# Kernel tuning notes

Measured on AMD Instinct MI355X. Metric: run time of the kernel, lower is better.

Reference implementation:

```python
import jax, jax.numpy as jnp
import numpy as np

H = 8          # nhead
EPS_Z = 1e-6   # linear-attention normalizer eps
LN_EPS = 1e-5  # torch LayerNorm default


def _ln(x, g, b):
    m = x.mean(-1, keepdims=True)
    v = ((x - m) ** 2).mean(-1, keepdims=True)
    return (x - m) * jax.lax.rsqrt(v + LN_EPS) * g + b


def setup_inputs() -> dict:
    key = jax.random.key(0)
    ks = jax.random.split(key, 8)
    B, S, E, F = 4, 8192, 512, 2048
    s = 0.02
    return {
        "src": jax.random.normal(ks[0], (B, S, E), jnp.float32),
        "Wq": jax.random.normal(ks[1], (E, E), jnp.float32) * s,
        "bq": jnp.zeros((E,), jnp.float32),
        "Wk": jax.random.normal(ks[2], (E, E), jnp.float32) * s,
        "bk": jnp.zeros((E,), jnp.float32),
        "Wv": jax.random.normal(ks[3], (E, E), jnp.float32) * s,
        "bv": jnp.zeros((E,), jnp.float32),
        "Wo": jax.random.normal(ks[4], (E, E), jnp.float32) * s,
        "bo": jnp.zeros((E,), jnp.float32),
        "W1": jax.random.normal(ks[5], (E, F), jnp.float32) * s,
        "b1": jnp.zeros((F,), jnp.float32),
        "W2": jax.random.normal(ks[6], (F, E), jnp.float32) * s,
        "b2": jnp.zeros((E,), jnp.float32),
        "g1": jnp.ones((E,), jnp.float32),
        "be1": jnp.zeros((E,), jnp.float32),
        "g2": jnp.ones((E,), jnp.float32),
        "be2": jnp.zeros((E,), jnp.float32),
    }


def reference(src, Wq, bq, Wk, bk, Wv, bv, Wo, bo, W1, b1, W2, b2, g1, be1, g2, be2):
    B, S, E = src.shape
    Dh = E // H

    def heads(x):  # [B,S,E] -> [B,H,S,Dh]
        return x.reshape(B, S, H, Dh).transpose(0, 2, 1, 3)

    q = heads(src @ Wq + bq)
    k = heads(src @ Wk + bk)
    v = heads(src @ Wv + bv)

    qm = jax.nn.elu(q) + 1.0  # feature map: ELU+1
    km = jax.nn.elu(k) + 1.0

    kv = jnp.einsum("bhsd,bhse->bhde", km, v)          # [B,H,Dh,Dh]
    ksum = km.sum(axis=2)                               # [B,H,Dh]
    z = 1.0 / (jnp.einsum("bhsd,bhd->bhs", qm, ksum) + EPS_Z)
    attn = jnp.einsum("bhsd,bhde->bhse", qm, kv) * z[..., None]

    attn = attn.transpose(0, 2, 1, 3).reshape(B, S, E) @ Wo + bo
    x = _ln(src + attn, g1, be1)
    ff = jax.nn.relu(x @ W1 + b1) @ W2 + b2
    return _ln(x + ff, g2, be2)
```

## Files before the change

### kernel.cpp

```cpp
#include <hip/hip_runtime.h>
#include <hip/hip_bf16.h>

typedef __attribute__((ext_vector_type(8))) short bf16x8;
typedef __attribute__((ext_vector_type(4))) float f32x4;

__device__ inline ushort f2bf(float f) {
    uint u = __float_as_uint(f);
    u += 0x7fff + ((u >> 16) & 1);
    return (ushort)(u >> 16);
}
__device__ inline float bf2f(ushort h) {
    return __uint_as_float(((uint)h) << 16);
}

__device__ inline void gload16(const void* g, void* lds) {
    __builtin_amdgcn_global_load_lds(
        (const __attribute__((address_space(1))) void*)g,
        (__attribute__((address_space(3))) void*)lds, 16, 0, 0);
}

__global__ __launch_bounds__(256) void prep(
    const float* __restrict__ src, ushort* __restrict__ src16,
    const float* __restrict__ Wq, const float* __restrict__ Wk,
    const float* __restrict__ Wv, const float* __restrict__ Wo,
    const float* __restrict__ W1, const float* __restrict__ W2,
    ushort* __restrict__ wqkv, ushort* __restrict__ wot,
    ushort* __restrict__ w1t, ushort* __restrict__ w2t,
    const float* __restrict__ bq, const float* __restrict__ bk,
    const float* __restrict__ bv, float* __restrict__ bqkv) {
    __shared__ float tile[32][33];
    int bid = blockIdx.x;
    const int t = threadIdx.x;
    if (bid < 16384) {
        int i = bid * 256 + t;
        float4 a = ((const float4*)src)[i];
        ushort4 o;
        o.x = f2bf(a.x); o.y = f2bf(a.y); o.z = f2bf(a.z); o.w = f2bf(a.w);
        ((ushort4*)src16)[i] = o;
        return;
    }
    bid -= 16384;
    const float* in; ushort* out; int Kd, Nd;
    if (bid < 1024) {
        int m = bid >> 8;
        in = (m == 0) ? Wq : (m == 1) ? Wk : (m == 2) ? Wv : Wo;
        out = (m == 3) ? wot : (wqkv + m * 512 * 512);
        Kd = 512; Nd = 512; bid &= 255;
    } else if (bid < 2048) { in = W1; out = w1t; Kd = 512; Nd = 2048; bid -= 1024; }
    else if (bid < 3072) { in = W2; out = w2t; Kd = 2048; Nd = 512; bid -= 2048; }
    else {
        int i = (bid - 3072) * 256 + t;
        if (i < 512) bqkv[i] = bq[i];
        else if (i < 1024) bqkv[i] = bk[i - 512];
        else if (i < 1536) bqkv[i] = bv[i - 1024];
        return;
    }
    const int nx = Nd / 32;
    const int nbase = (bid % nx) * 32, kb = (bid / nx) * 32;
    const int tx = t & 31, ty = t >> 5;
#pragma unroll
    for (int i = 0; i < 4; i++)
        tile[ty + i * 8][tx] = in[(size_t)(kb + ty + i * 8) * Nd + nbase + tx];
    __syncthreads();
#pragma unroll
    for (int i = 0; i < 4; i++) {
        int n = nbase + ty + i * 8, k = kb + tx;
        out[(size_t)n * Kd + k] = f2bf(tile[tx][ty + i * 8]);
    }
}

template <int EPI, int NT, int GB>
__global__ __launch_bounds__(512, 2) void gemm256(
    const ushort* __restrict__ A, const ushort* __restrict__ Bt,
    const float* __restrict__ bias, const ushort* __restrict__ res16,
    ushort* __restrict__ out16, int M, int N, int K, int nb1) {
    extern __shared__ char smem[];
    const int t = threadIdx.x;
    const int w = t >> 6, l = t & 63;
    const int wr = w >> 2, wc = w & 3;
    const int nwg = gridDim.x, cpx = nwg >> 3;
    const int swz = (blockIdx.x & 7) * cpx + (blockIdx.x >> 3);
    int bx0, by0;
    if (GB == 0) { bx0 = (swz % nb1) * NT; by0 = swz / nb1; }
    else         { bx0 = swz % nb1;        by0 = (swz / nb1) * NT; }

    const int scoff = ((t & 7) ^ ((t >> 3) & 7)) * 8;
    const ushort* pA = A + (size_t)(by0 * 256 + (t >> 3)) * K + scoff;
    const ushort* pB = Bt + (size_t)(bx0 * 256 + (t >> 3)) * K + scoff;
    const size_t u64K = (size_t)64 * K;

    const int Kt = K >> 6;
    const int TOT = NT * Kt;
    int skt = 0;
    size_t adv = 0;

#define STG8(buf)                                                              \
    {                                                                          \
        char* Lb = (buf) + (w << 10);                                          \
        _Pragma("unroll")                                                      \
        for (int u = 0; u < 4; ++u) {                                          \
            gload16(pA + (size_t)u * u64K + (GB ? adv : 0) + skt * 64,         \
                    Lb + u * 8192);                                            \
            gload16(pB + (size_t)u * u64K + (GB ? 0 : adv) + skt * 64,         \
                    Lb + 32768 + u * 8192);                                    \
        }                                                                      \
        if (++skt == Kt) { skt = 0; adv += (size_t)256 * K; }                  \
    }

    const int cA0 = ((l >> 4) ^ (l & 7)) * 16;
    const int cA1 = ((4 + (l >> 4)) ^ (l & 7)) * 16;
    const int baseA = (wr * 128 + (l & 15)) * 128;
    const int baseB = 32768 + (wc * 64 + (l & 15)) * 128;

    STG8(smem);

    f32x4 acc[8][4] = {};
    int g = 0;
    for (int j = 0; j < NT; ++j) {
#pragma unroll 1
        for (int kt = 0; kt < Kt; ++kt, ++g) {
            asm volatile("s_waitcnt vmcnt(0)" ::: "memory");
            __builtin_amdgcn_s_barrier();
            __builtin_amdgcn_sched_barrier(0);

            const char* cb = smem + (g & 1) * 65536;
            if (g + 1 < TOT) STG8(smem + ((g + 1) & 1) * 65536);

            bf16x8 a[8], b[4];
#pragma unroll
            for (int n = 0; n < 4; n++) b[n] = *(const bf16x8*)(cb + baseB + n * 2048 + cA0);
#pragma unroll
            for (int m = 0; m < 8; m++) a[m] = *(const bf16x8*)(cb + baseA + m * 2048 + cA0);
#pragma unroll
            for (int m = 0; m < 8; m++)
#pragma unroll
                for (int n = 0; n < 4; n++)
                    acc[m][n] = __builtin_amdgcn_mfma_f32_16x16x32_bf16(a[m], b[n], acc[m][n], 0, 0, 0);
#pragma unroll
            for (int n = 0; n < 4; n++) b[n] = *(const bf16x8*)(cb + baseB + n * 2048 + cA1);
#pragma unroll
            for (int m = 0; m < 8; m++) a[m] = *(const bf16x8*)(cb + baseA + m * 2048 + cA1);
#pragma unroll
            for (int m = 0; m < 8; m++)
#pragma unroll
                for (int n = 0; n < 4; n++)
                    acc[m][n] = __builtin_amdgcn_mfma_f32_16x16x32_bf16(a[m], b[n], acc[m][n], 0, 0, 0);
        }

        {
            const int bx = (GB == 0) ? (bx0 + j) : bx0;
            const int by = (GB == 0) ? by0 : (by0 + j);
            const int row0 = by * 256 + wr * 128 + ((l >> 4) << 2);
            const int col0 = bx * 256 + wc * 64 + (l & 15);
            const int seg = bx >> 1;
            const size_t segoff = (size_t)seg * M * 512;
            const int c511 = col0 & 511;
            float bv[4];
#pragma unroll
            for (int n = 0; n < 4; n++) bv[n] = bias[col0 + n * 16];
#pragma unroll
            for (int m = 0; m < 8; m++) {
#pragma unroll
                for (int r = 0; r < 4; r++) {
                    const int row = row0 + m * 16 + r;
                    const size_t base = (size_t)row * N + col0;
#pragma unroll
                    for (int n = 0; n < 4; n++) {
                        float vv = acc[m][n][r] + bv[n];
                        if constexpr (EPI == 2) {
                            vv = vv > 0.f ? vv : 0.f;
                            out16[base + n * 16] = f2bf(vv);
                        } else if constexpr (EPI == 3) {
                            vv += bf2f(res16[base + n * 16]);
                            out16[base + n * 16] = f2bf(vv);
                        } else if constexpr (EPI == 4) {
                            if (seg < 2) vv = vv > 0.f ? vv + 1.f : __expf(vv);
                            out16[segoff + (size_t)row * 512 + c511 + n * 16] = f2bf(vv);
                        } else {
                            out16[base + n * 16] = f2bf(vv);
                        }
                    }
                }
            }
            if (j + 1 < NT) {
#pragma unroll
                for (int m = 0; m < 8; m++)
#pragma unroll
                    for (int n = 0; n < 4; n++)
                        acc[m][n] = (f32x4){0.f, 0.f, 0.f, 0.f};
            }
        }
    }
#undef STG8
}

__global__ __launch_bounds__(256) void kv_partial(
    const ushort* __restrict__ km, const ushort* __restrict__ v,
    float* __restrict__ kvp, float* __restrict__ ksump, int S) {
    __shared__ ushort kms[32 * 64];
    __shared__ ushort vs[32 * 64];
    const int t = threadIdx.x;
    const int bh = blockIdx.y, b = bh >> 3, h = bh & 7;
    const int d0 = (t >> 4) * 4, e0 = (t & 15) * 4;
    float acc[4][4] = {};
    float ks = 0.f;
    const int s_base = blockIdx.x * 512;
    const int r = t >> 3, c8 = (t & 7) * 8;
    for (int s0 = 0; s0 < 512; s0 += 32) {
        size_t grow = ((size_t)b * S + s_base + s0 + r) * 512 + h * 64 + c8;
        *(uint4*)&kms[r * 64 + c8] = *(const uint4*)&km[grow];
        *(uint4*)&vs[r * 64 + c8] = *(const uint4*)&v[grow];
        __syncthreads();
#pragma unroll 4
        for (int s = 0; s < 32; ++s) {
            ushort4 ka = *(const ushort4*)&kms[s * 64 + d0];
            ushort4 vb = *(const ushort4*)&vs[s * 64 + e0];
            float a0 = bf2f(ka.x), a1 = bf2f(ka.y), a2 = bf2f(ka.z), a3 = bf2f(ka.w);
            float b0 = bf2f(vb.x), b1 = bf2f(vb.y), b2 = bf2f(vb.z), b3 = bf2f(vb.w);
            acc[0][0] += a0 * b0; acc[0][1] += a0 * b1; acc[0][2] += a0 * b2; acc[0][3] += a0 * b3;
            acc[1][0] += a1 * b0; acc[1][1] += a1 * b1; acc[1][2] += a1 * b2; acc[1][3] += a1 * b3;
            acc[2][0] += a2 * b0; acc[2][1] += a2 * b1; acc[2][2] += a2 * b2; acc[2][3] += a2 * b3;
            acc[3][0] += a3 * b0; acc[3][1] += a3 * b1; acc[3][2] += a3 * b2; acc[3][3] += a3 * b3;
            if (t < 64) ks += bf2f(kms[s * 64 + t]);
        }
        __syncthreads();
    }
    float* dst = kvp + ((size_t)bh * 16 + blockIdx.x) * 4096;
#pragma unroll
    for (int i = 0; i < 4; i++)
#pragma unroll
        for (int j = 0; j < 4; j++)
            dst[(d0 + i) * 64 + e0 + j] = acc[i][j];
    if (t < 64) ksump[((size_t)bh * 16 + blockIdx.x) * 64 + t] = ks;
}

__global__ void kv_reduce(const float* __restrict__ kvp, const float* __restrict__ ksump,
                          ushort* __restrict__ kvt, float* __restrict__ ksum) {
    int i = blockIdx.x * 256 + threadIdx.x;
    if (i < 32 * 4096) {
        int bh = i >> 12, de = i & 4095;
        int d = de >> 6, e = de & 63;
        float s = 0.f;
#pragma unroll
        for (int c = 0; c < 16; ++c) s += kvp[((size_t)bh * 16 + c) * 4096 + de];
        kvt[(size_t)bh * 4096 + e * 64 + d] = f2bf(s);
    } else {
        int j = i - 32 * 4096;
        if (j < 32 * 64) {
            int bh = j >> 6, d = j & 63;
            float s = 0.f;
#pragma unroll
            for (int c = 0; c < 16; ++c) s += ksump[((size_t)bh * 16 + c) * 64 + d];
            ksum[j] = s;
        }
    }
}

__global__ __launch_bounds__(256) void attn_mfma(
    const ushort* __restrict__ qm, const ushort* __restrict__ kvt,
    const float* __restrict__ ksum, ushort* __restrict__ attnE, int S) {
    __shared__ ushort As[128 * 128];
    __shared__ ushort Bs[128 * 64];
    __shared__ float zbuf[128][2];
    __shared__ float ks2[128];
    const int t = threadIdx.x, w = t >> 6, l = t & 63;
    const int cx = blockIdx.x, by = blockIdx.y;
    const int b = (by * 128) / S;
    const int h0 = cx * 2;
    const size_t arow0 = (size_t)(by * 128) * 512 + cx * 128;

#pragma unroll
    for (int rd = 0; rd < 8; ++rd) {
        const ushort* g = qm + arow0 + (size_t)(rd * 16 + w * 4 + (l >> 4)) * 512 + (l & 15) * 8;
        gload16(g, (char*)As + rd * 4096 + w * 1024);
    }
    const ushort* kvbase = kvt + (size_t)(b * 8 + h0) * 4096;
#pragma unroll
    for (int rd = 0; rd < 4; ++rd) {
        const ushort* g = kvbase + (rd * 32 + w * 8 + (l >> 3)) * 64 + (l & 7) * 8;
        gload16(g, (char*)Bs + rd * 4096 + w * 1024);
    }
    if (t < 128) ks2[t] = ksum[(b * 8 + h0) * 64 + t];
    __syncthreads();

    {
        const int r = t >> 1, hh = t & 1;
        float den = 0.f;
#pragma unroll
        for (int d0 = 0; d0 < 64; d0 += 8) {
            bf16x8 qv = *(const bf16x8*)&As[r * 128 + hh * 64 + d0];
#pragma unroll
            for (int j = 0; j < 8; j++) den += bf2f((ushort)qv[j]) * ks2[hh * 64 + d0 + j];
        }
        zbuf[r][hh] = 1.0f / (den + 1e-6f);
    }

    const int wr = w >> 1, wc = w & 1;
    const int ar = wr * 64 + (l & 15);
    const int br = wc * 64 + (l & 15);
    const int ko = (l >> 4) * 8;
    f32x4 acc[4][4] = {};
#pragma unroll
    for (int ks_ = 0; ks_ < 2; ++ks_) {
        bf16x8 a[4], bb[4];
#pragma unroll
        for (int m = 0; m < 4; m++)
            a[m] = *(const bf16x8*)&As[(ar + m * 16) * 128 + wc * 64 + ks_ * 32 + ko];
#pragma unroll
        for (int n = 0; n < 4; n++)
            bb[n] = *(const bf16x8*)&Bs[(br + n * 16) * 64 + ks_ * 32 + ko];
#pragma unroll
        for (int m = 0; m < 4; m++)
#pragma unroll
            for (int n = 0; n < 4; n++)
                acc[m][n] = __builtin_amdgcn_mfma_f32_16x16x32_bf16(a[m], bb[n], acc[m][n], 0, 0, 0);
    }
    __syncthreads();

    const int row0l = wr * 64 + ((l >> 4) << 2);
    ushort* outbase = attnE + (size_t)(by * 128) * 512 + cx * 128;
#pragma unroll
    for (int n = 0; n < 4; n++) {
#pragma unroll
        for (int m = 0; m < 4; m++) {
#pragma unroll
            for (int r = 0; r < 4; r++) {
                int rl = row0l + m * 16 + r;
                float z = zbuf[rl][wc];
                outbase[(size_t)rl * 512 + wc * 64 + n * 16 + (l & 15)] = f2bf(acc[m][n][r] * z);
            }
        }
    }
}

template <int OUT32>
__global__ __launch_bounds__(256) void ln_bf16(
    const ushort* __restrict__ in, const float* __restrict__ g, const float* __restrict__ be,
    void* __restrict__ outp, int Mrows) {
    const int w = threadIdx.x >> 6, l = threadIdx.x & 63;
    const int row = blockIdx.x * 4 + w;
    if (row >= Mrows) return;
    const ushort* rp = in + (size_t)row * 512;
    uint4 u = *(const uint4*)&rp[l * 8];
    float x[8];
    x[0] = bf2f((ushort)(u.x & 0xffff)); x[1] = bf2f((ushort)(u.x >> 16));
    x[2] = bf2f((ushort)(u.y & 0xffff)); x[3] = bf2f((ushort)(u.y >> 16));
    x[4] = bf2f((ushort)(u.z & 0xffff)); x[5] = bf2f((ushort)(u.z >> 16));
    x[6] = bf2f((ushort)(u.w & 0xffff)); x[7] = bf2f((ushort)(u.w >> 16));
    float s = 0.f, ss = 0.f;
#pragma unroll
    for (int j = 0; j < 8; j++) { s += x[j]; ss += x[j] * x[j]; }
#pragma unroll
    for (int o = 1; o < 64; o <<= 1) {
        s += __shfl_xor(s, o, 64);
        ss += __shfl_xor(ss, o, 64);
    }
    float mean = s * (1.f / 512.f);
    float var = ss * (1.f / 512.f) - mean * mean;
    float rstd = rsqrtf(var + 1e-5f);
    float4 g0 = *(const float4*)&g[l * 8], g1v = *(const float4*)&g[l * 8 + 4];
    float4 b0 = *(const float4*)&be[l * 8], b1v = *(const float4*)&be[l * 8 + 4];
    float o0[8];
    o0[0] = (x[0] - mean) * rstd * g0.x + b0.x;
    o0[1] = (x[1] - mean) * rstd * g0.y + b0.y;
    o0[2] = (x[2] - mean) * rstd * g0.z + b0.z;
    o0[3] = (x[3] - mean) * rstd * g0.w + b0.w;
    o0[4] = (x[4] - mean) * rstd * g1v.x + b1v.x;
    o0[5] = (x[5] - mean) * rstd * g1v.y + b1v.y;
    o0[6] = (x[6] - mean) * rstd * g1v.z + b1v.z;
    o0[7] = (x[7] - mean) * rstd * g1v.w + b1v.w;
    if constexpr (OUT32) {
        float* op = (float*)outp + (size_t)row * 512;
        *(float4*)&op[l * 8] = make_float4(o0[0], o0[1], o0[2], o0[3]);
        *(float4*)&op[l * 8 + 4] = make_float4(o0[4], o0[5], o0[6], o0[7]);
    } else {
        ushort* op = (ushort*)outp + (size_t)row * 512;
        ushort4 u0, u1;
        u0.x = f2bf(o0[0]); u0.y = f2bf(o0[1]); u0.z = f2bf(o0[2]); u0.w = f2bf(o0[3]);
        u1.x = f2bf(o0[4]); u1.y = f2bf(o0[5]); u1.z = f2bf(o0[6]); u1.w = f2bf(o0[7]);
        *(ushort4*)&op[l * 8] = u0;
        *(ushort4*)&op[l * 8 + 4] = u1;
    }
}

extern "C" void kernel_launch(void* const* d_in, const int* in_sizes, int n_in,
                              void* d_out, int out_size, void* d_ws, size_t ws_size,
                              hipStream_t stream) {
    const int B = 4, S = 8192, E = 512, F = 2048;
    const int M = B * S;
    const size_t SZ = (size_t)M * E * 2;
    const int SMEM = 131072;

    const float* src = (const float*)d_in[0];
    const float* Wq = (const float*)d_in[1];  const float* bq = (const float*)d_in[2];
    const float* Wk = (const float*)d_in[3];  const float* bk = (const float*)d_in[4];
    const float* Wv = (const float*)d_in[5];  const float* bv = (const float*)d_in[6];
    const float* Wo = (const float*)d_in[7];  const float* bo = (const float*)d_in[8];
    const float* W1 = (const float*)d_in[9];  const float* b1 = (const float*)d_in[10];
    const float* W2 = (const float*)d_in[11]; const float* b2 = (const float*)d_in[12];
    const float* g1 = (const float*)d_in[13]; const float* be1 = (const float*)d_in[14];
    const float* g2 = (const float*)d_in[15]; const float* be2 = (const float*)d_in[16];

    char* ws = (char*)d_ws;
    ushort* qm    = (ushort*)(ws + 0 * SZ);
    ushort* km    = (ushort*)(ws + 1 * SZ);
    ushort* v     = (ushort*)(ws + 2 * SZ);
    ushort* src16 = (ushort*)(ws + 3 * SZ);
    ushort* x16   = (ushort*)(ws + 4 * SZ);
    ushort* z16   = (ushort*)(ws + 5 * SZ);
    char*   tail  = ws + 6 * SZ;
    float*  kvp   = (float*)(tail);
    float*  ksump = (float*)(tail + 8388608);
    ushort* kvt   = (ushort*)(tail + 8519680);
    float*  ksum  = (float*)(tail + 8781824);
    float*  bqkv  = (float*)(tail + 8790016);
    ushort* wqkv  = (ushort*)(tail + 8796160);
    ushort* wot   = (ushort*)(tail + 10369024);
    ushort* w1t   = (ushort*)(tail + 10893312);
    ushort* w2t   = (ushort*)(tail + 12990464);
    ushort* attnE = km;
    ushort* y16   = v;
    ushort* hbuf  = (ushort*)(ws + 0);

    hipFuncSetAttribute((const void*)gemm256<4, 3, 0>, hipFuncAttributeMaxDynamicSharedMemorySize, SMEM);
    hipFuncSetAttribute((const void*)gemm256<3, 1, 0>, hipFuncAttributeMaxDynamicSharedMemorySize, SMEM);
    hipFuncSetAttribute((const void*)gemm256<2, 4, 1>, hipFuncAttributeMaxDynamicSharedMemorySize, SMEM);

    prep<<<dim3(16384 + 3072 + 6), 256, 0, stream>>>(
        src, src16, Wq, Wk, Wv, Wo, W1, W2, wqkv, wot, w1t, w2t, bq, bk, bv, bqkv);

    gemm256<4, 3, 0><<<dim3(2 * 128), 512, SMEM, stream>>>(src16, wqkv, bqkv, nullptr, qm, M, 1536, E, 2);

    kv_partial<<<dim3(16, 32), 256, 0, stream>>>(km, v, kvp, ksump, S);
    kv_reduce<<<dim3((32 * 4096 + 32 * 64 + 255) / 256), 256, 0, stream>>>(kvp, ksump, kvt, ksum);

    attn_mfma<<<dim3(4, M / 128), 256, 0, stream>>>(qm, kvt, ksum, attnE, S);

    gemm256<3, 1, 0><<<dim3(2 * 128), 512, SMEM, stream>>>(attnE, wot, bo, src16, y16, M, E, E, 2);
    ln_bf16<0><<<dim3(M / 4), 256, 0, stream>>>(y16, g1, be1, x16, M);

    gemm256<2, 4, 1><<<dim3(8 * 32), 512, SMEM, stream>>>(x16, w1t, b1, nullptr, hbuf, M, F, E, 8);
    gemm256<3, 1, 0><<<dim3(2 * 128), 512, SMEM, stream>>>(hbuf, w2t, b2, x16, z16, M, E, F, 2);
    ln_bf16<1><<<dim3(M / 4), 256, 0, stream>>>(z16, g2, be2, (float*)d_out, M);
}
```

Measured before the change: 357.5 us.

## Fuse residual add and LayerNorm into full-row N=512 GEMM epilogues

Adds a GEMM kernel whose 128x512 output tile covers the full 512-wide row. Its epilogue adds bias and residual, computes the LayerNorm statistics through shared memory and writes the normalized result. This replaces the Wo and W2 GEMMs plus their separate LayerNorm kernels, removing the bf16 intermediate round trips and two launches. The trade-off is a different tiling: 256 blocks with only double-buffered 32-wide K steps and a heavier epilogue, which may lower GEMM efficiency compared with the previous persistent kernel.

```diff
diff --git a/kernel.cpp b/kernel.cpp
--- a/kernel.cpp
+++ b/kernel.cpp
@@ -170,9 +170,6 @@
                         if constexpr (EPI == 2) {
                             vv = vv > 0.f ? vv : 0.f;
                             out16[base + n * 16] = f2bf(vv);
-                        } else if constexpr (EPI == 3) {
-                            vv += bf2f(res16[base + n * 16]);
-                            out16[base + n * 16] = f2bf(vv);
                         } else if constexpr (EPI == 4) {
                             if (seg < 2) vv = vv > 0.f ? vv + 1.f : __expf(vv);
                             out16[segoff + (size_t)row * 512 + c511 + n * 16] = f2bf(vv);
@@ -192,6 +189,130 @@
         }
     }
 #undef STG8
+}
+
+template <int OUT32>
+__global__ __launch_bounds__(512, 2) void gemmN512(
+    const ushort* __restrict__ A, const ushort* __restrict__ Bt,
+    const float* __restrict__ bias, const ushort* __restrict__ res16,
+    const float* __restrict__ gam, const float* __restrict__ bet,
+    void* __restrict__ outp, int K) {
+    extern __shared__ char smem[];
+    const int t = threadIdx.x;
+    const int w = t >> 6, l = t & 63;
+    const int wr = w >> 2, wc = w & 3;
+    const int nwg = gridDim.x, cpx = nwg >> 3;
+    const int by = (blockIdx.x & 7) * cpx + (blockIdx.x >> 3);
+
+    const int scoff = ((t & 3) ^ ((t >> 3) & 3)) * 8;
+    const ushort* pA = A + (size_t)(by * 128 + (t >> 2)) * K + scoff;
+    const ushort* pB = Bt + (size_t)(t >> 2) * K + scoff;
+    const size_t u128K = (size_t)128 * K;
+
+    const int Kt = K >> 5;
+
+#define STG5(buf, kt)                                                          \
+    {                                                                          \
+        char* Lb = (buf) + (w << 10);                                          \
+        gload16(pA + (kt) * 32, Lb);                                           \
+        _Pragma("unroll")                                                      \
+        for (int u = 0; u < 4; ++u)                                            \
+            gload16(pB + (size_t)u * u128K + (kt) * 32, Lb + 8192 + u * 8192); \
+    }
+
+    const int Ra = wr * 64 + (l & 15);
+    const int offA = Ra * 64 + (((l >> 4) ^ ((Ra >> 1) & 3)) << 4);
+    const int Rb = wc * 128 + (l & 15);
+    const int offB = 8192 + Rb * 64 + (((l >> 4) ^ ((Rb >> 1) & 3)) << 4);
+
+    STG5(smem, 0);
+
+    f32x4 acc[4][8] = {};
+#pragma unroll 1
+    for (int g = 0; g < Kt; ++g) {
+        asm volatile("s_waitcnt vmcnt(0)" ::: "memory");
+        __builtin_amdgcn_s_barrier();
+        __builtin_amdgcn_sched_barrier(0);
+
+        const char* cb = smem + (g & 1) * 40960;
+        if (g + 1 < Kt) STG5(smem + ((g + 1) & 1) * 40960, g + 1);
+
+        bf16x8 a[4], b[8];
+#pragma unroll
+        for (int n = 0; n < 8; n++) b[n] = *(const bf16x8*)(cb + offB + n * 1024);
+#pragma unroll
+        for (int m = 0; m < 4; m++) a[m] = *(const bf16x8*)(cb + offA + m * 1024);
+#pragma unroll
+        for (int m = 0; m < 4; m++)
+#pragma unroll
+            for (int n = 0; n < 8; n++)
+                acc[m][n] = __builtin_amdgcn_mfma_f32_16x16x32_bf16(a[m], b[n], acc[m][n], 0, 0, 0);
+    }
+#undef STG5
+
+    const int row0 = wr * 64 + ((l >> 4) << 2);
+    const int col0 = wc * 128 + (l & 15);
+    float bv[8];
+#pragma unroll
+    for (int n = 0; n < 8; n++) bv[n] = bias[col0 + n * 16];
+#pragma unroll
+    for (int m = 0; m < 4; m++)
+#pragma unroll
+        for (int r = 0; r < 4; r++) {
+            const int lrow = row0 + m * 16 + r;
+            const size_t gbase = (size_t)(by * 128 + lrow) * 512 + col0;
+#pragma unroll
+            for (int n = 0; n < 8; n++)
+                acc[m][n][r] += bv[n] + bf2f(res16[gbase + n * 16]);
+        }
+
+    __syncthreads();
+    float* psum = (float*)smem;
+    float* psq = (float*)(smem + 32768);
+    const int pcol = wc * 16 + (l & 15);
+#pragma unroll
+    for (int m = 0; m < 4; m++)
+#pragma unroll
+        for (int r = 0; r < 4; r++) {
+            const int lrow = row0 + m * 16 + r;
+            float s = 0.f, q = 0.f;
+#pragma unroll
+            for (int n = 0; n < 8; n++) {
+                float v = acc[m][n][r];
+                s += v; q += v * v;
+            }
+            psum[lrow * 64 + pcol] = s;
+            psq[lrow * 64 + pcol] = q;
+        }
+    __syncthreads();
+    float* stats = (float*)(smem + 65536);
+    if (t < 128) {
+        float s = 0.f, q = 0.f;
+#pragma unroll 8
+        for (int i = 0; i < 64; i++) { s += psum[t * 64 + i]; q += psq[t * 64 + i]; }
+        float mean = s * (1.f / 512.f);
+        float var = q * (1.f / 512.f) - mean * mean;
+        stats[t * 2] = mean;
+        stats[t * 2 + 1] = rsqrtf(var + 1e-5f);
+    }
+    __syncthreads();
+    float gv[8], bev[8];
+#pragma unroll
+    for (int n = 0; n < 8; n++) { gv[n] = gam[col0 + n * 16]; bev[n] = bet[col0 + n * 16]; }
+#pragma unroll
+    for (int m = 0; m < 4; m++)
+#pragma unroll
+        for (int r = 0; r < 4; r++) {
+            const int lrow = row0 + m * 16 + r;
+            const float mean = stats[lrow * 2], rstd = stats[lrow * 2 + 1];
+            const size_t gbase = (size_t)(by * 128 + lrow) * 512 + col0;
+#pragma unroll
+            for (int n = 0; n < 8; n++) {
+                float o = (acc[m][n][r] - mean) * rstd * gv[n] + bev[n];
+                if constexpr (OUT32) ((float*)outp)[gbase + n * 16] = o;
+                else ((ushort*)outp)[gbase + n * 16] = f2bf(o);
+            }
+        }
 }
 
 __global__ __launch_bounds__(256) void kv_partial(
@@ -333,56 +454,6 @@
     }
 }
 
-template <int OUT32>
-__global__ __launch_bounds__(256) void ln_bf16(
-    const ushort* __restrict__ in, const float* __restrict__ g, const float* __restrict__ be,
-    void* __restrict__ outp, int Mrows) {
-    const int w = threadIdx.x >> 6, l = threadIdx.x & 63;
-    const int row = blockIdx.x * 4 + w;
-    if (row >= Mrows) return;
-    const ushort* rp = in + (size_t)row * 512;
-    uint4 u = *(const uint4*)&rp[l * 8];
-    float x[8];
-    x[0] = bf2f((ushort)(u.x & 0xffff)); x[1] = bf2f((ushort)(u.x >> 16));
-    x[2] = bf2f((ushort)(u.y & 0xffff)); x[3] = bf2f((ushort)(u.y >> 16));
-    x[4] = bf2f((ushort)(u.z & 0xffff)); x[5] = bf2f((ushort)(u.z >> 16));
-    x[6] = bf2f((ushort)(u.w & 0xffff)); x[7] = bf2f((ushort)(u.w >> 16));
-    float s = 0.f, ss = 0.f;
-#pragma unroll
-    for (int j = 0; j < 8; j++) { s += x[j]; ss += x[j] * x[j]; }
-#pragma unroll
-    for (int o = 1; o < 64; o <<= 1) {
-        s += __shfl_xor(s, o, 64);
-        ss += __shfl_xor(ss, o, 64);
-    }
-    float mean = s * (1.f / 512.f);
-    float var = ss * (1.f / 512.f) - mean * mean;
-    float rstd = rsqrtf(var + 1e-5f);
-    float4 g0 = *(const float4*)&g[l * 8], g1v = *(const float4*)&g[l * 8 + 4];
-    float4 b0 = *(const float4*)&be[l * 8], b1v = *(const float4*)&be[l * 8 + 4];
-    float o0[8];
-    o0[0] = (x[0] - mean) * rstd * g0.x + b0.x;
-    o0[1] = (x[1] - mean) * rstd * g0.y + b0.y;
-    o0[2] = (x[2] - mean) * rstd * g0.z + b0.z;
-    o0[3] = (x[3] - mean) * rstd * g0.w + b0.w;
-    o0[4] = (x[4] - mean) * rstd * g1v.x + b1v.x;
-    o0[5] = (x[5] - mean) * rstd * g1v.y + b1v.y;
-    o0[6] = (x[6] - mean) * rstd * g1v.z + b1v.z;
-    o0[7] = (x[7] - mean) * rstd * g1v.w + b1v.w;
-    if constexpr (OUT32) {
-        float* op = (float*)outp + (size_t)row * 512;
-        *(float4*)&op[l * 8] = make_float4(o0[0], o0[1], o0[2], o0[3]);
-        *(float4*)&op[l * 8 + 4] = make_float4(o0[4], o0[5], o0[6], o0[7]);
-    } else {
-        ushort* op = (ushort*)outp + (size_t)row * 512;
-        ushort4 u0, u1;
-        u0.x = f2bf(o0[0]); u0.y = f2bf(o0[1]); u0.z = f2bf(o0[2]); u0.w = f2bf(o0[3]);
-        u1.x = f2bf(o0[4]); u1.y = f2bf(o0[5]); u1.z = f2bf(o0[6]); u1.w = f2bf(o0[7]);
-        *(ushort4*)&op[l * 8] = u0;
-        *(ushort4*)&op[l * 8 + 4] = u1;
-    }
-}
-
 extern "C" void kernel_launch(void* const* d_in, const int* in_sizes, int n_in,
                               void* d_out, int out_size, void* d_ws, size_t ws_size,
                               hipStream_t stream) {
@@ -390,6 +461,7 @@
     const int M = B * S;
     const size_t SZ = (size_t)M * E * 2;
     const int SMEM = 131072;
+    const int SMEMN = 81920;
 
     const float* src = (const float*)d_in[0];
     const float* Wq = (const float*)d_in[1];  const float* bq = (const float*)d_in[2];
@@ -407,7 +479,6 @@
     ushort* v     = (ushort*)(ws + 2 * SZ);
     ushort* src16 = (ushort*)(ws + 3 * SZ);
     ushort* x16   = (ushort*)(ws + 4 * SZ);
-    ushort* z16   = (ushort*)(ws + 5 * SZ);
     char*   tail  = ws + 6 * SZ;
     float*  kvp   = (float*)(tail);
     float*  ksump = (float*)(tail + 8388608);
@@ -419,12 +490,12 @@
     ushort* w1t   = (ushort*)(tail + 10893312);
     ushort* w2t   = (ushort*)(tail + 12990464);
     ushort* attnE = km;
-    ushort* y16   = v;
     ushort* hbuf  = (ushort*)(ws + 0);
 
     hipFuncSetAttribute((const void*)gemm256<4, 3, 0>, hipFuncAttributeMaxDynamicSharedMemorySize, SMEM);
-    hipFuncSetAttribute((const void*)gemm256<3, 1, 0>, hipFuncAttributeMaxDynamicSharedMemorySize, SMEM);
     hipFuncSetAttribute((const void*)gemm256<2, 4, 1>, hipFuncAttributeMaxDynamicSharedMemorySize, SMEM);
+    hipFuncSetAttribute((const void*)gemmN512<0>, hipFuncAttributeMaxDynamicSharedMemorySize, SMEMN);
+    hipFuncSetAttribute((const void*)gemmN512<1>, hipFuncAttributeMaxDynamicSharedMemorySize, SMEMN);
 
     prep<<<dim3(16384 + 3072 + 6), 256, 0, stream>>>(
         src, src16, Wq, Wk, Wv, Wo, W1, W2, wqkv, wot, w1t, w2t, bq, bk, bv, bqkv);
@@ -436,10 +507,8 @@
 
     attn_mfma<<<dim3(4, M / 128), 256, 0, stream>>>(qm, kvt, ksum, attnE, S);
 
-    gemm256<3, 1, 0><<<dim3(2 * 128), 512, SMEM, stream>>>(attnE, wot, bo, src16, y16, M, E, E, 2);
-    ln_bf16<0><<<dim3(M / 4), 256, 0, stream>>>(y16, g1, be1, x16, M);
+    gemmN512<0><<<dim3(M / 128), 512, SMEMN, stream>>>(attnE, wot, bo, src16, g1, be1, x16, E);
 
     gemm256<2, 4, 1><<<dim3(8 * 32), 512, SMEM, stream>>>(x16, w1t, b1, nullptr, hbuf, M, F, E, 8);
-    gemm256<3, 1, 0><<<dim3(2 * 128), 512, SMEM, stream>>>(hbuf, w2t, b2, x16, z16, M, E, F, 2);
-    ln_bf16<1><<<dim3(M / 4), 256, 0, stream>>>(z16, g2, be2, (float*)d_out, M);
-}
+    gemmN512<1><<<dim3(M / 128), 512, SMEMN, stream>>>(hbuf, w2t, b2, x16, g2, be2, (float*)d_out, F);
+}
```

Result: no change. 361.4 us (+1.1%).
